# Kernel optimization log

Hardware: AMD Instinct MI355X
Metric: run time of the kernel (lower is better)

Reference implementation:

```python
import jax, jax.numpy as jnp
import numpy as np

LN_EPS = 1e-5
N_HEADS = 8

def _layernorm(x, g, b):
    mu = jnp.mean(x, axis=-1, keepdims=True)
    var = jnp.var(x, axis=-1, keepdims=True)
    return (x - mu) * jax.lax.rsqrt(var + LN_EPS) * g + b

def _posenc(seqlen, d_model, dtype):
    den = jnp.exp(-jnp.arange(0, d_model, 2, dtype=dtype) * (np.log(10000.0) / d_model))
    pos = jnp.arange(seqlen, dtype=dtype)[:, None]  # [S,1]
    pe = jnp.zeros((seqlen, d_model), dtype=dtype)
    pe = pe.at[:, 0::2].set(jnp.sin(pos * den))
    pe = pe.at[:, 1::2].set(jnp.cos(pos * den)[:, : d_model // 2])
    return pe  # [S,d]

def setup_inputs() -> dict:
    key = jax.random.key(0)
    ks = jax.random.split(key, 12)
    B, S, V, D, F, L, DL = 64, 256, 16, 512, 2048, 6, 256
    s = 0.05
    return {
        "src_pad": jax.random.normal(ks[0], (B, S, V), jnp.float32),
        "emb_w": jax.random.normal(ks[1], (D, V), jnp.float32) * s,
        "emb_b": jnp.zeros((D,), jnp.float32),
        "qkv_w": jax.random.normal(ks[2], (L, 3 * D, D), jnp.float32) * s,
        "qkv_b": jnp.zeros((L, 3 * D), jnp.float32),
        "out_w": jax.random.normal(ks[3], (L, D, D), jnp.float32) * s,
        "out_b": jnp.zeros((L, D), jnp.float32),
        "ff1_w": jax.random.normal(ks[4], (L, F, D), jnp.float32) * s,
        "ff1_b": jnp.zeros((L, F), jnp.float32),
        "ff2_w": jax.random.normal(ks[5], (L, D, F), jnp.float32) * s,
        "ff2_b": jnp.zeros((L, D), jnp.float32),
        "ln1_g": jnp.ones((L, D), jnp.float32),
        "ln1_b": jnp.zeros((L, D), jnp.float32),
        "ln2_g": jnp.ones((L, D), jnp.float32),
        "ln2_b": jnp.zeros((L, D), jnp.float32),
        "lat_w": jax.random.normal(ks[6], (DL, S * D), jnp.float32) * 0.005,
        "lat_b": jnp.zeros((DL,), jnp.float32),
        "head_w": jax.random.normal(ks[7], (1, DL), jnp.float32) * s,
        "head_b": jnp.zeros((1,), jnp.float32),
    }

def reference(src_pad, emb_w, emb_b, qkv_w, qkv_b, out_w, out_b,
              ff1_w, ff1_b, ff2_w, ff2_b, ln1_g, ln1_b, ln2_g, ln2_b,
              lat_w, lat_b, head_w, head_b):
    B, S, V = src_pad.shape
    D = emb_w.shape[0]
    L = qkv_w.shape[0]
    H = N_HEADS
    dh = D // H
    # batched replacement of the per-token Python-loop embedding
    x = jnp.einsum('bsv,dv->bsd', src_pad, emb_w) + emb_b
    x = x + _posenc(S, D, x.dtype)  # dropout is identity at eval
    scale = 1.0 / np.sqrt(dh)
    for l in range(L):  # post-norm PyTorch TransformerEncoderLayer, relu FFN
        qkv = jnp.einsum('bsd,ed->bse', x, qkv_w[l]) + qkv_b[l]  # [B,S,3D]
        q, k, v = jnp.split(qkv, 3, axis=-1)
        q = q.reshape(B, S, H, dh).transpose(0, 2, 1, 3)
        k = k.reshape(B, S, H, dh).transpose(0, 2, 1, 3)
        v = v.reshape(B, S, H, dh).transpose(0, 2, 1, 3)
        attn = jax.nn.softmax(jnp.einsum('bhqd,bhkd->bhqk', q, k) * scale, axis=-1)
        o = jnp.einsum('bhqk,bhkd->bhqd', attn, v).transpose(0, 2, 1, 3).reshape(B, S, D)
        o = jnp.einsum('bsd,ed->bse', o, out_w[l]) + out_b[l]
        x = _layernorm(x + o, ln1_g[l], ln1_b[l])
        h = jax.nn.relu(jnp.einsum('bsd,fd->bsf', x, ff1_w[l]) + ff1_b[l])
        h = jnp.einsum('bsf,df->bsd', h, ff2_w[l]) + ff2_b[l]
        x = _layernorm(x + h, ln2_g[l], ln2_b[l])
    mem = x.reshape(B, S * D) @ lat_w.T + lat_b  # [B, d_latent]
    pred = jax.nn.sigmoid(mem @ head_w.T + head_b)  # [B,1]
    return pred
```

## Files before the change

kernel.cpp:

```cpp
#include <hip/hip_runtime.h>
#include <hip/hip_bf16.h>
#include <cstdint>

#define DEV static __device__ __forceinline__

typedef __attribute__((ext_vector_type(8))) short bf16x8;
typedef __attribute__((ext_vector_type(4))) float f32x4;

DEV unsigned short f2bf(float f) {
  union { float f; unsigned u; } c; c.f = f;
  unsigned u = c.u;
  return (unsigned short)((u + 0x7fffu + ((u >> 16) & 1u)) >> 16);
}
DEV float bf2f(unsigned short h) {
  union { unsigned u; float f; } c; c.u = ((unsigned)h) << 16; return c.f;
}
DEV float bflo(unsigned u) { union { unsigned u; float f; } c; c.u = u << 16; return c.f; }
DEV float bfhi(unsigned u) { union { unsigned u; float f; } c; c.u = u & 0xffff0000u; return c.f; }
DEV unsigned pack_bf16(float a, float b) {
  union { float f; unsigned u; } ca, cb; ca.f = a; cb.f = b;
  return __builtin_amdgcn_perm(cb.u + 0x8000u, ca.u + 0x8000u, 0x07060302u);
}

#define ASYNC_COPY16(gsrc, ldst)                                                      \
  __builtin_amdgcn_global_load_lds(                                                   \
      (const __attribute__((address_space(1))) void*)(unsigned long long)(gsrc),      \
      (__attribute__((address_space(3))) void*)(unsigned int)(unsigned long long)(ldst), \
      16, 0, 0)

__global__ void cvt_all_kernel(const float* __restrict__ s0, unsigned short* __restrict__ d0,
                               const float* __restrict__ s1, unsigned short* __restrict__ d1,
                               const float* __restrict__ s2, unsigned short* __restrict__ d2,
                               const float* __restrict__ s3, unsigned short* __restrict__ d3) {
  const int blk = blockIdx.x;
  const float* s; unsigned short* d; int base;
  if (blk < 4608)       { s = s0; d = d0; base = blk; }
  else if (blk < 6144)  { s = s1; d = d1; base = blk - 4608; }
  else if (blk < 12288) { s = s2; d = d2; base = blk - 6144; }
  else                  { s = s3; d = d3; base = blk - 12288; }
  size_t i = ((size_t)base * 256 + threadIdx.x) * 4;
  float4 v = *(const float4*)(s + i);
  d[i + 0] = f2bf(v.x);
  d[i + 1] = f2bf(v.y);
  d[i + 2] = f2bf(v.z);
  d[i + 3] = f2bf(v.w);
}

__global__ void embed_kernel(const float* __restrict__ src,
                             const float* __restrict__ emb_w,
                             const float* __restrict__ emb_b,
                             unsigned short* __restrict__ xb) {
  const int bs = blockIdx.x;
  const int d = threadIdx.x;
  const int s = bs & 255;
  __shared__ float sv[16];
  if (d < 16) sv[d] = src[(size_t)bs * 16 + d];
  __syncthreads();
  const float* wr = emb_w + (size_t)d * 16;
  float acc = emb_b[d];
#pragma unroll
  for (int v = 0; v < 16; v++) acc += sv[v] * wr[v];
  const float den = __expf(-(float)(d & ~1) * (9.2103403719761836f / 512.f));
  const float arg = (float)s * den;
  acc += (d & 1) ? __cosf(arg) : __sinf(arg);
  xb[(size_t)bs * 512 + d] = f2bf(acc);
}

template <int BM, int RELU>
__global__ __launch_bounds__(512, 2) void gemm_pipe(
    const unsigned short* __restrict__ A,
    const unsigned short* __restrict__ B,
    const float* __restrict__ bias,
    unsigned short* __restrict__ Cb,
    int M, int N, int K) {
  constexpr int BN = 256;
  constexpr int MT = BM / 32;
  constexpr int NT = 4;
  constexpr int NLA = BM / 64;
  constexpr int NL = NLA + BN / 64;
  constexpr int BUFE = (BM + BN) * 64;
  __shared__ unsigned short lds[3 * BUFE];

  const int tid = threadIdx.x;
  const int lane = tid & 63;
  const int w = tid >> 6;
  const int wmi = w >> 2;
  const int wni = w & 3;
  const int r16 = lane & 15;
  const int quad = lane >> 4;
  const int rsw = r16 & 7;
  const int m0 = blockIdx.x * BM;
  const int n0 = blockIdx.y * BN;

  const int srow = tid >> 3;
  const int scol = ((tid & 7) ^ (srow & 7)) * 8;
  const unsigned short* gA = A + (size_t)(m0 + srow) * K + scol;
  const unsigned short* gB = B + (size_t)(n0 + srow) * K + scol;

#define STG(i, bufi, kc)                                                        \
  do {                                                                          \
    if ((i) < NLA)                                                              \
      ASYNC_COPY16(gA + (size_t)((i) * 64) * K + (kc),                          \
                   lds + (bufi) * BUFE + ((i) * 64 + w * 8) * 64);              \
    else                                                                        \
      ASYNC_COPY16(gB + (size_t)(((i) - NLA) * 64) * K + (kc),                  \
                   lds + (bufi) * BUFE + (BM + ((i) - NLA) * 64 + w * 8) * 64); \
  } while (0)

  f32x4 acc[MT][NT] = {};

  const int NK = K >> 6;
#pragma unroll
  for (int i = 0; i < NL; ++i) STG(i, 0, 0);
#pragma unroll
  for (int i = 0; i < NL; ++i) STG(i, 1, 64);

  for (int kt = 0; kt < NK; ++kt) {
    const int buf = kt % 3;
    if (kt + 1 < NK)
      asm volatile("s_waitcnt vmcnt(%0)" ::"i"(NL) : "memory");
    else
      asm volatile("s_waitcnt vmcnt(0)" ::: "memory");
    __builtin_amdgcn_s_barrier();
    if (kt + 2 < NK) {
      const int sb = (kt + 2) % 3;
      const int kc = (kt + 2) << 6;
#pragma unroll
      for (int i = 0; i < NL; ++i) STG(i, sb, kc);
    }
    const unsigned short* As = lds + buf * BUFE;
    const unsigned short* Bs = As + BM * 64;
#pragma unroll
    for (int kh = 0; kh < 2; ++kh) {
      const int ko = ((kh * 4 + quad) ^ rsw) * 8;
      bf16x8 aR[MT], bR[NT];
#pragma unroll
      for (int m = 0; m < MT; ++m)
        aR[m] = *(const bf16x8*)(As + (wmi * 64 + m * 16 + r16) * 64 + ko);
#pragma unroll
      for (int j = 0; j < NT; ++j)
        bR[j] = *(const bf16x8*)(Bs + (wni * 64 + j * 16 + r16) * 64 + ko);
      __builtin_amdgcn_s_setprio(1);
#pragma unroll
      for (int m = 0; m < MT; ++m)
#pragma unroll
        for (int j = 0; j < NT; ++j)
          acc[m][j] = __builtin_amdgcn_mfma_f32_16x16x32_bf16(
              bR[j], aR[m], acc[m][j], 0, 0, 0);
      __builtin_amdgcn_s_setprio(0);
    }
    asm volatile("s_waitcnt lgkmcnt(0)" ::: "memory");
  }
#undef STG

  const int mb = m0 + wmi * 64 + r16;
  const int nb = n0 + wni * 64 + quad * 4;
#pragma unroll
  for (int j = 0; j < NT; ++j) {
    const int n = nb + j * 16;
    const float4 bv = *(const float4*)(bias + n);
#pragma unroll
    for (int i = 0; i < MT; ++i) {
      const size_t off = (size_t)(mb + i * 16) * N + n;
      float4 v;
      v.x = acc[i][j][0] + bv.x;
      v.y = acc[i][j][1] + bv.y;
      v.z = acc[i][j][2] + bv.z;
      v.w = acc[i][j][3] + bv.w;
      if (RELU) {
        v.x = fmaxf(v.x, 0.f); v.y = fmaxf(v.y, 0.f);
        v.z = fmaxf(v.z, 0.f); v.w = fmaxf(v.w, 0.f);
      }
      uint2 u;
      u.x = pack_bf16(v.x, v.y);
      u.y = pack_bf16(v.z, v.w);
      *(uint2*)(Cb + off) = u;
    }
  }
}

__global__ __launch_bounds__(512, 2) void gemm_ln(
    const unsigned short* __restrict__ A,
    const unsigned short* __restrict__ B,
    const float* __restrict__ bias,
    const float* __restrict__ g,
    const float* __restrict__ beta,
    unsigned short* __restrict__ xb,
    int K) {
  constexpr int BM = 64;
  constexpr int MT = 4;
  constexpr int NT = 4;
  constexpr int NL = 1 + 8;
  constexpr int BUFE = (BM + 512) * 64;
  __shared__ unsigned short lds[2 * BUFE];

  const int tid = threadIdx.x;
  const int lane = tid & 63;
  const int w = tid >> 6;
  const int r16 = lane & 15;
  const int quad = lane >> 4;
  const int rsw = r16 & 7;
  const int m0 = blockIdx.x * BM;

  const int srow = tid >> 3;
  const int scol = ((tid & 7) ^ (srow & 7)) * 8;
  const unsigned short* gA = A + (size_t)(m0 + srow) * K + scol;
  const unsigned short* gB = B + (size_t)srow * K + scol;

#define STG2(i, bufi, kc)                                                       \
  do {                                                                          \
    if ((i) == 0)                                                               \
      ASYNC_COPY16(gA + (size_t)(kc), lds + (bufi) * BUFE + (w * 8) * 64);      \
    else                                                                        \
      ASYNC_COPY16(gB + (size_t)(((i) - 1) * 64) * K + (kc),                    \
                   lds + (bufi) * BUFE + (BM + ((i) - 1) * 64 + w * 8) * 64);   \
  } while (0)

  f32x4 acc[MT][NT] = {};

  const int NK = K >> 6;
#pragma unroll
  for (int i = 0; i < NL; ++i) STG2(i, 0, 0);

  for (int kt = 0; kt < NK; ++kt) {
    const int buf = kt & 1;
    if (kt + 1 < NK) {
      const int kc = (kt + 1) << 6;
#pragma unroll
      for (int i = 0; i < NL; ++i) STG2(i, buf ^ 1, kc);
      asm volatile("s_waitcnt vmcnt(%0)" ::"i"(NL) : "memory");
    } else {
      asm volatile("s_waitcnt vmcnt(0)" ::: "memory");
    }
    __builtin_amdgcn_s_barrier();
    const unsigned short* As = lds + buf * BUFE;
    const unsigned short* Bs = As + BM * 64;
#pragma unroll
    for (int kh = 0; kh < 2; ++kh) {
      const int ko = ((kh * 4 + quad) ^ rsw) * 8;
      bf16x8 aR[MT], bR[NT];
#pragma unroll
      for (int m = 0; m < MT; ++m)
        aR[m] = *(const bf16x8*)(As + (m * 16 + r16) * 64 + ko);
#pragma unroll
      for (int j = 0; j < NT; ++j)
        bR[j] = *(const bf16x8*)(Bs + (w * 64 + j * 16 + r16) * 64 + ko);
      __builtin_amdgcn_s_setprio(1);
#pragma unroll
      for (int m = 0; m < MT; ++m)
#pragma unroll
        for (int j = 0; j < NT; ++j)
          acc[m][j] = __builtin_amdgcn_mfma_f32_16x16x32_bf16(
              bR[j], aR[m], acc[m][j], 0, 0, 0);
      __builtin_amdgcn_s_setprio(0);
    }
    asm volatile("s_waitcnt lgkmcnt(0)" ::: "memory");
    __builtin_amdgcn_s_barrier();
  }
#undef STG2

  const int nb = w * 64 + quad * 4;
  float psum[MT] = {}, psq[MT] = {};
#pragma unroll
  for (int j = 0; j < NT; ++j) {
    const int n = nb + j * 16;
    const float4 bv = *(const float4*)(bias + n);
#pragma unroll
    for (int i = 0; i < MT; ++i) {
      const size_t off = (size_t)(m0 + i * 16 + r16) * 512 + n;
      const uint2 ru = *(const uint2*)(xb + off);
      f32x4 v;
      v[0] = acc[i][j][0] + bv.x + bflo(ru.x);
      v[1] = acc[i][j][1] + bv.y + bfhi(ru.x);
      v[2] = acc[i][j][2] + bv.z + bflo(ru.y);
      v[3] = acc[i][j][3] + bv.w + bfhi(ru.y);
      acc[i][j] = v;
#pragma unroll
      for (int r = 0; r < 4; ++r) {
        psum[i] += v[r];
        psq[i] += v[r] * v[r];
      }
    }
  }
#pragma unroll
  for (int i = 0; i < MT; ++i) {
    psum[i] += __shfl_xor(psum[i], 16);
    psum[i] += __shfl_xor(psum[i], 32);
    psq[i] += __shfl_xor(psq[i], 16);
    psq[i] += __shfl_xor(psq[i], 32);
  }
  float* redS = (float*)lds;
  float* redQ = redS + 512;
  if (quad == 0) {
#pragma unroll
    for (int i = 0; i < MT; ++i) {
      redS[w * 64 + i * 16 + r16] = psum[i];
      redQ[w * 64 + i * 16 + r16] = psq[i];
    }
  }
  __syncthreads();
  float mu[MT], rs[MT];
#pragma unroll
  for (int i = 0; i < MT; ++i) {
    const int row = i * 16 + r16;
    float s = 0.f, q = 0.f;
#pragma unroll
    for (int ww = 0; ww < 8; ++ww) {
      s += redS[ww * 64 + row];
      q += redQ[ww * 64 + row];
    }
    mu[i] = s * (1.f / 512.f);
    rs[i] = rsqrtf(q * (1.f / 512.f) - mu[i] * mu[i] + 1e-5f);
  }
#pragma unroll
  for (int j = 0; j < NT; ++j) {
    const int n = nb + j * 16;
    const float4 gv = *(const float4*)(g + n);
    const float4 be = *(const float4*)(beta + n);
#pragma unroll
    for (int i = 0; i < MT; ++i) {
      const size_t off = (size_t)(m0 + i * 16 + r16) * 512 + n;
      const f32x4 v = acc[i][j];
      float o0 = (v[0] - mu[i]) * rs[i] * gv.x + be.x;
      float o1 = (v[1] - mu[i]) * rs[i] * gv.y + be.y;
      float o2 = (v[2] - mu[i]) * rs[i] * gv.z + be.z;
      float o3 = (v[3] - mu[i]) * rs[i] * gv.w + be.w;
      uint2 u;
      u.x = pack_bf16(o0, o1);
      u.y = pack_bf16(o2, o3);
      *(uint2*)(xb + off) = u;
    }
  }
}

__global__ __launch_bounds__(256, 2) void attn_fused(
    const unsigned short* __restrict__ qkv,
    unsigned short* __restrict__ O) {
  __shared__ unsigned short Vt[64 * 264];
  __shared__ unsigned short Pl[32 * 264];
  __shared__ float redM[4][32];
  __shared__ float redS[4][32];
  const int tid = threadIdx.x;
  const int lane = tid & 63;
  const int w = tid >> 6;
  const int r16 = lane & 15;
  const int quad = lane >> 4;
  const int h = blockIdx.x & 7;
  const int b = blockIdx.x >> 3;

  {
    const int kp = w * 32 + (lane & 31);
    const int dhalf = lane >> 5;
    const unsigned short* vbase =
        qkv + (size_t)(b * 256 + 2 * kp) * 1536 + 1024 + h * 64;
    unsigned* dst = (unsigned*)Vt;
#pragma unroll
    for (int t = 0; t < 4; t++) {
      const int dc = dhalf + 2 * t;
      const uint4 a = *(const uint4*)(vbase + dc * 8);
      const uint4 bb = *(const uint4*)(vbase + 1536 + dc * 8);
      const unsigned* ap = (const unsigned*)&a;
      const unsigned* bp = (const unsigned*)&bb;
#pragma unroll
      for (int i = 0; i < 4; i++) {
        const unsigned lo = ap[i], hi = bp[i];
        dst[(dc * 8 + 2 * i) * 132 + kp] = (lo & 0xffffu) | (hi << 16);
        dst[(dc * 8 + 2 * i + 1) * 132 + kp] = (lo >> 16) | (hi & 0xffff0000u);
      }
    }
  }
  __syncthreads();

  const unsigned short* krow =
      qkv + (size_t)(b * 256 + r16) * 1536 + 512 + h * 64 + quad * 8;
  const unsigned short* qrow =
      qkv + (size_t)(b * 256 + r16) * 1536 + h * 64 + quad * 8;

  for (int qt = 0; qt < 8; qt++) {
    const int q0 = qt * 32;
    f32x4 acc[4][2] = {};
    bf16x8 bQ0[2], bQ1[2];
#pragma unroll
    for (int nt = 0; nt < 2; nt++) {
      const unsigned short* qp = qrow + (size_t)(q0 + nt * 16) * 1536;
      bQ0[nt] = *(const bf16x8*)(qp);
      bQ1[nt] = *(const bf16x8*)(qp + 32);
    }
#pragma unroll
    for (int mt = 0; mt < 4; mt++) {
      const unsigned short* kp = krow + (size_t)(w * 64 + mt * 16) * 1536;
      const bf16x8 aK0 = *(const bf16x8*)(kp);
      const bf16x8 aK1 = *(const bf16x8*)(kp + 32);
#pragma unroll
      for (int nt = 0; nt < 2; nt++) {
        acc[mt][nt] = __builtin_amdgcn_mfma_f32_16x16x32_bf16(aK0, bQ0[nt], acc[mt][nt], 0, 0, 0);
        acc[mt][nt] = __builtin_amdgcn_mfma_f32_16x16x32_bf16(aK1, bQ1[nt], acc[mt][nt], 0, 0, 0);
      }
    }
    float ml[2];
#pragma unroll
    for (int nt = 0; nt < 2; nt++) {
      float m = acc[0][nt][0];
#pragma unroll
      for (int mt = 0; mt < 4; mt++)
#pragma unroll
        for (int r = 0; r < 4; r++) m = fmaxf(m, acc[mt][nt][r]);
      m = fmaxf(m, __shfl_xor(m, 16));
      m = fmaxf(m, __shfl_xor(m, 32));
      ml[nt] = m;
      float s = 0.f;
#pragma unroll
      for (int mt = 0; mt < 4; mt++)
#pragma unroll
        for (int r = 0; r < 4; r++) {
          acc[mt][nt][r] = __expf((acc[mt][nt][r] - m) * 0.125f);
          s += acc[mt][nt][r];
        }
      s += __shfl_xor(s, 16);
      s += __shfl_xor(s, 32);
      if (quad == 0) {
        redM[w][nt * 16 + r16] = m;
        redS[w][nt * 16 + r16] = s;
      }
    }
    __syncthreads();
    float scale[2];
#pragma unroll
    for (int nt = 0; nt < 2; nt++) {
      const int q = nt * 16 + r16;
      const float m0_ = redM[0][q], m1_ = redM[1][q];
      const float m2_ = redM[2][q], m3_ = redM[3][q];
      const float mg = fmaxf(fmaxf(m0_, m1_), fmaxf(m2_, m3_));
      const float sg = redS[0][q] * __expf((m0_ - mg) * 0.125f) +
                       redS[1][q] * __expf((m1_ - mg) * 0.125f) +
                       redS[2][q] * __expf((m2_ - mg) * 0.125f) +
                       redS[3][q] * __expf((m3_ - mg) * 0.125f);
      scale[nt] = __expf((ml[nt] - mg) * 0.125f) / sg;
    }
#pragma unroll
    for (int nt = 0; nt < 2; nt++) {
      unsigned short* prow = Pl + (nt * 16 + r16) * 264 + w * 64 + quad * 4;
#pragma unroll
      for (int mt = 0; mt < 4; mt++) {
        uint2 u;
        u.x = pack_bf16(acc[mt][nt][0] * scale[nt], acc[mt][nt][1] * scale[nt]);
        u.y = pack_bf16(acc[mt][nt][2] * scale[nt], acc[mt][nt][3] * scale[nt]);
        *(uint2*)(prow + mt * 16) = u;
      }
    }
    __syncthreads();
    f32x4 o[2] = {};
#pragma unroll
    for (int s = 0; s < 8; s++) {
      const bf16x8 aV = *(const bf16x8*)(Vt + (w * 16 + r16) * 264 + s * 32 + quad * 8);
#pragma unroll
      for (int nt = 0; nt < 2; nt++) {
        const bf16x8 bP = *(const bf16x8*)(Pl + (nt * 16 + r16) * 264 + s * 32 + quad * 8);
        o[nt] = __builtin_amdgcn_mfma_f32_16x16x32_bf16(aV, bP, o[nt], 0, 0, 0);
      }
    }
#pragma unroll
    for (int nt = 0; nt < 2; nt++) {
      uint2 u;
      u.x = pack_bf16(o[nt][0], o[nt][1]);
      u.y = pack_bf16(o[nt][2], o[nt][3]);
      *(uint2*)(O + (size_t)(b * 256 + q0 + nt * 16 + r16) * 512 + h * 64 +
                w * 16 + quad * 4) = u;
    }
  }
}

__global__ void zero_kernel(float* __restrict__ p) {
  p[blockIdx.x * 256 + threadIdx.x] = 0.f;
}

__global__ __launch_bounds__(256) void latent_gemm(
    const unsigned short* __restrict__ xb, const float* __restrict__ W,
    float* __restrict__ mem) {
  const int tid = threadIdx.x;
  const int lane = tid & 63;
  const int w = tid >> 6;
  const int r16 = lane & 15;
  const int quad = lane >> 4;
  const int n0 = blockIdx.x * 64 + w * 16;
  const int kc0 = blockIdx.y * 1024;

  const float* wrow = W + (size_t)(n0 + r16) * 131072 + kc0 + quad * 8;
  const unsigned short* xrow = xb + (size_t)r16 * 131072 + kc0 + quad * 8;

  f32x4 c[4] = {};
  for (int k = 0; k < 1024; k += 32) {
    const float4 wa = *(const float4*)(wrow + k);
    const float4 wb = *(const float4*)(wrow + k + 4);
    union { unsigned u[4]; bf16x8 v; } cw;
    cw.u[0] = pack_bf16(wa.x, wa.y);
    cw.u[1] = pack_bf16(wa.z, wa.w);
    cw.u[2] = pack_bf16(wb.x, wb.y);
    cw.u[3] = pack_bf16(wb.z, wb.w);
#pragma unroll
    for (int i = 0; i < 4; i++) {
      const bf16x8 aX = *(const bf16x8*)(xrow + (size_t)i * 2097152 + k);
      c[i] = __builtin_amdgcn_mfma_f32_16x16x32_bf16(aX, cw.v, c[i], 0, 0, 0);
    }
  }
#pragma unroll
  for (int i = 0; i < 4; i++)
#pragma unroll
    for (int r = 0; r < 4; r++)
      atomicAdd(&mem[(size_t)(i * 16 + quad * 4 + r) * 256 + n0 + r16], c[i][r]);
}

__global__ __launch_bounds__(256) void head_kernel(
    const float* __restrict__ mem, const float* __restrict__ lat_b,
    const float* __restrict__ head_w, const float* __restrict__ head_b,
    float* __restrict__ out) {
  const int b = blockIdx.x;
  const int tid = threadIdx.x;
  float v = (mem[(size_t)b * 256 + tid] + lat_b[tid]) * head_w[tid];
#pragma unroll
  for (int off = 32; off > 0; off >>= 1) v += __shfl_xor(v, off);
  __shared__ float red[4];
  const int w = tid >> 6, lane = tid & 63;
  if (lane == 0) red[w] = v;
  __syncthreads();
  if (tid == 0) {
    const float z = red[0] + red[1] + red[2] + red[3] + head_b[0];
    out[b] = 1.f / (1.f + __expf(-z));
  }
}

extern "C" void kernel_launch(void* const* d_in, const int* in_sizes, int n_in,
                              void* d_out, int out_size, void* d_ws, size_t ws_size,
                              hipStream_t stream) {
  (void)in_sizes; (void)n_in; (void)out_size; (void)ws_size;
  const float* src_pad = (const float*)d_in[0];
  const float* emb_w = (const float*)d_in[1];
  const float* emb_b = (const float*)d_in[2];
  const float* qkv_w = (const float*)d_in[3];
  const float* qkv_b = (const float*)d_in[4];
  const float* out_w = (const float*)d_in[5];
  const float* out_b = (const float*)d_in[6];
  const float* ff1_w = (const float*)d_in[7];
  const float* ff1_b = (const float*)d_in[8];
  const float* ff2_w = (const float*)d_in[9];
  const float* ff2_b = (const float*)d_in[10];
  const float* ln1_g = (const float*)d_in[11];
  const float* ln1_b = (const float*)d_in[12];
  const float* ln2_g = (const float*)d_in[13];
  const float* ln2_b = (const float*)d_in[14];
  const float* lat_w = (const float*)d_in[15];
  const float* lat_b = (const float*)d_in[16];
  const float* head_w = (const float*)d_in[17];
  const float* head_b = (const float*)d_in[18];
  float* out = (float*)d_out;

  char* p = (char*)d_ws;
  unsigned short* xb = (unsigned short*)p; p += (size_t)16384 * 512 * 2;
  unsigned short* qkv = (unsigned short*)p; p += (size_t)16384 * 1536 * 2;
  unsigned short* attno = (unsigned short*)p; p += (size_t)16384 * 512 * 2;
  unsigned short* h = (unsigned short*)p;     p += (size_t)16384 * 2048 * 2;
  unsigned short* wq = (unsigned short*)p;    p += (size_t)4718592 * 2;
  unsigned short* wo = (unsigned short*)p;    p += (size_t)1572864 * 2;
  unsigned short* wf1 = (unsigned short*)p;   p += (size_t)6291456 * 2;
  unsigned short* wf2 = (unsigned short*)p;   p += (size_t)6291456 * 2;
  float* mem = (float*)p;           p += (size_t)16384 * 4;

  cvt_all_kernel<<<18432, 256, 0, stream>>>(qkv_w, wq, out_w, wo, ff1_w, wf1,
                                            ff2_w, wf2);

  embed_kernel<<<16384, 512, 0, stream>>>(src_pad, emb_w, emb_b, xb);

  for (int l = 0; l < 6; l++) {
    gemm_pipe<128, 0><<<dim3(128, 6), 512, 0, stream>>>(
        xb, wq + (size_t)l * 786432, qkv_b + (size_t)l * 1536, qkv,
        16384, 1536, 512);
    attn_fused<<<512, 256, 0, stream>>>(qkv, attno);
    gemm_ln<<<256, 512, 0, stream>>>(
        attno, wo + (size_t)l * 262144, out_b + (size_t)l * 512,
        ln1_g + (size_t)l * 512, ln1_b + (size_t)l * 512, xb, 512);
    gemm_pipe<128, 1><<<dim3(128, 8), 512, 0, stream>>>(
        xb, wf1 + (size_t)l * 1048576, ff1_b + (size_t)l * 2048, h,
        16384, 2048, 512);
    gemm_ln<<<256, 512, 0, stream>>>(
        h, wf2 + (size_t)l * 1048576, ff2_b + (size_t)l * 512,
        ln2_g + (size_t)l * 512, ln2_b + (size_t)l * 512, xb, 2048);
  }

  zero_kernel<<<64, 256, 0, stream>>>(mem);
  latent_gemm<<<dim3(4, 128), 256, 0, stream>>>(xb, lat_w, mem);
  head_kernel<<<64, 256, 0, stream>>>(mem, lat_b, head_w, head_b, out);
}
```

Measured before the change: 1.511 ms.

## Replace triple-buffered 128x256 GEMM with simple single-buffered 128x128 GEMM

Replaces the pipelined GEMM with a simpler kernel for the QKV and FF1 projections. The old kernel used three LDS stages and async prefetch two tiles ahead over a 128x256 tile with 512 threads. The new kernel uses a 128x128 tile, 256 threads and a single LDS buffer that is loaded, waited on and synchronised every k-step. The intent is higher occupancy and more blocks, at the cost of losing the overlap of global loads with MFMA work and getting less reuse of A per block.

Result: faster. 1.477 ms (-2.3%).

```diff
diff --git a/kernel.cpp b/kernel.cpp
--- a/kernel.cpp
+++ b/kernel.cpp
@@ -66,101 +66,74 @@
   xb[(size_t)bs * 512 + d] = f2bf(acc);
 }
 
-template <int BM, int RELU>
-__global__ __launch_bounds__(512, 2) void gemm_pipe(
+template <int RELU>
+__global__ __launch_bounds__(256, 3) void gemm_nt(
     const unsigned short* __restrict__ A,
     const unsigned short* __restrict__ B,
     const float* __restrict__ bias,
     unsigned short* __restrict__ Cb,
     int M, int N, int K) {
-  constexpr int BN = 256;
-  constexpr int MT = BM / 32;
+  constexpr int MT = 4;
   constexpr int NT = 4;
-  constexpr int NLA = BM / 64;
-  constexpr int NL = NLA + BN / 64;
-  constexpr int BUFE = (BM + BN) * 64;
-  __shared__ unsigned short lds[3 * BUFE];
-
+  __shared__ unsigned short As[128 * 64];
+  __shared__ unsigned short Bs[128 * 64];
   const int tid = threadIdx.x;
   const int lane = tid & 63;
   const int w = tid >> 6;
-  const int wmi = w >> 2;
-  const int wni = w & 3;
+  const int m0 = blockIdx.x * 128;
+  const int n0 = blockIdx.y * 128;
+
+  const int srow = lane >> 3;
+  const int scol = (((lane & 7) ^ srow)) * 8;
+  const unsigned short* gA0 = A + (size_t)(m0 + w * 32 + srow) * K + scol;
+  unsigned short* lA0 = As + (w * 32) * 64;
+  const unsigned short* gB0 = B + (size_t)(n0 + w * 32 + srow) * K + scol;
+  unsigned short* lB0 = Bs + (w * 32) * 64;
+
+  const int wm = (w >> 1) * 64;
+  const int wn = (w & 1) * 64;
   const int r16 = lane & 15;
   const int quad = lane >> 4;
   const int rsw = r16 & 7;
-  const int m0 = blockIdx.x * BM;
-  const int n0 = blockIdx.y * BN;
-
-  const int srow = tid >> 3;
-  const int scol = ((tid & 7) ^ (srow & 7)) * 8;
-  const unsigned short* gA = A + (size_t)(m0 + srow) * K + scol;
-  const unsigned short* gB = B + (size_t)(n0 + srow) * K + scol;
-
-#define STG(i, bufi, kc)                                                        \
-  do {                                                                          \
-    if ((i) < NLA)                                                              \
-      ASYNC_COPY16(gA + (size_t)((i) * 64) * K + (kc),                          \
-                   lds + (bufi) * BUFE + ((i) * 64 + w * 8) * 64);              \
-    else                                                                        \
-      ASYNC_COPY16(gB + (size_t)(((i) - NLA) * 64) * K + (kc),                  \
-                   lds + (bufi) * BUFE + (BM + ((i) - NLA) * 64 + w * 8) * 64); \
-  } while (0)
 
   f32x4 acc[MT][NT] = {};
 
-  const int NK = K >> 6;
-#pragma unroll
-  for (int i = 0; i < NL; ++i) STG(i, 0, 0);
-#pragma unroll
-  for (int i = 0; i < NL; ++i) STG(i, 1, 64);
-
-  for (int kt = 0; kt < NK; ++kt) {
-    const int buf = kt % 3;
-    if (kt + 1 < NK)
-      asm volatile("s_waitcnt vmcnt(%0)" ::"i"(NL) : "memory");
-    else
-      asm volatile("s_waitcnt vmcnt(0)" ::: "memory");
-    __builtin_amdgcn_s_barrier();
-    if (kt + 2 < NK) {
-      const int sb = (kt + 2) % 3;
-      const int kc = (kt + 2) << 6;
-#pragma unroll
-      for (int i = 0; i < NL; ++i) STG(i, sb, kc);
-    }
-    const unsigned short* As = lds + buf * BUFE;
-    const unsigned short* Bs = As + BM * 64;
-#pragma unroll
-    for (int kh = 0; kh < 2; ++kh) {
+  for (int k0 = 0; k0 < K; k0 += 64) {
+#pragma unroll
+    for (int i = 0; i < 4; i++)
+      ASYNC_COPY16(gA0 + (size_t)(i * 8) * K + k0, lA0 + i * 512);
+#pragma unroll
+    for (int i = 0; i < 4; i++)
+      ASYNC_COPY16(gB0 + (size_t)(i * 8) * K + k0, lB0 + i * 512);
+    asm volatile("s_waitcnt vmcnt(0)" ::: "memory");
+    __syncthreads();
+#pragma unroll
+    for (int kh = 0; kh < 2; kh++) {
       const int ko = ((kh * 4 + quad) ^ rsw) * 8;
-      bf16x8 aR[MT], bR[NT];
-#pragma unroll
-      for (int m = 0; m < MT; ++m)
-        aR[m] = *(const bf16x8*)(As + (wmi * 64 + m * 16 + r16) * 64 + ko);
-#pragma unroll
-      for (int j = 0; j < NT; ++j)
-        bR[j] = *(const bf16x8*)(Bs + (wni * 64 + j * 16 + r16) * 64 + ko);
-      __builtin_amdgcn_s_setprio(1);
-#pragma unroll
-      for (int m = 0; m < MT; ++m)
-#pragma unroll
-        for (int j = 0; j < NT; ++j)
-          acc[m][j] = __builtin_amdgcn_mfma_f32_16x16x32_bf16(
-              bR[j], aR[m], acc[m][j], 0, 0, 0);
-      __builtin_amdgcn_s_setprio(0);
-    }
-    asm volatile("s_waitcnt lgkmcnt(0)" ::: "memory");
-  }
-#undef STG
-
-  const int mb = m0 + wmi * 64 + r16;
-  const int nb = n0 + wni * 64 + quad * 4;
-#pragma unroll
-  for (int j = 0; j < NT; ++j) {
+      bf16x8 xa[MT], wb[NT];
+#pragma unroll
+      for (int i = 0; i < MT; i++)
+        xa[i] = *(const bf16x8*)(As + (wm + i * 16 + r16) * 64 + ko);
+#pragma unroll
+      for (int j = 0; j < NT; j++)
+        wb[j] = *(const bf16x8*)(Bs + (wn + j * 16 + r16) * 64 + ko);
+#pragma unroll
+      for (int i = 0; i < MT; i++)
+#pragma unroll
+        for (int j = 0; j < NT; j++)
+          acc[i][j] = __builtin_amdgcn_mfma_f32_16x16x32_bf16(wb[j], xa[i], acc[i][j], 0, 0, 0);
+    }
+    __syncthreads();
+  }
+
+  const int mb = m0 + wm + r16;
+  const int nb = n0 + wn + quad * 4;
+#pragma unroll
+  for (int j = 0; j < NT; j++) {
     const int n = nb + j * 16;
     const float4 bv = *(const float4*)(bias + n);
 #pragma unroll
-    for (int i = 0; i < MT; ++i) {
+    for (int i = 0; i < MT; i++) {
       const size_t off = (size_t)(mb + i * 16) * N + n;
       float4 v;
       v.x = acc[i][j][0] + bv.x;
@@ -571,14 +544,14 @@
   embed_kernel<<<16384, 512, 0, stream>>>(src_pad, emb_w, emb_b, xb);
 
   for (int l = 0; l < 6; l++) {
-    gemm_pipe<128, 0><<<dim3(128, 6), 512, 0, stream>>>(
+    gemm_nt<0><<<dim3(128, 12), 256, 0, stream>>>(
         xb, wq + (size_t)l * 786432, qkv_b + (size_t)l * 1536, qkv,
         16384, 1536, 512);
     attn_fused<<<512, 256, 0, stream>>>(qkv, attno);
     gemm_ln<<<256, 512, 0, stream>>>(
         attno, wo + (size_t)l * 262144, out_b + (size_t)l * 512,
         ln1_g + (size_t)l * 512, ln1_b + (size_t)l * 512, xb, 512);
-    gemm_pipe<128, 1><<<dim3(128, 8), 512, 0, stream>>>(
+    gemm_nt<1><<<dim3(128, 16), 256, 0, stream>>>(
         xb, wf1 + (size_t)l * 1048576, ff1_b + (size_t)l * 2048, h,
         16384, 2048, 512);
     gemm_ln<<<256, 512, 0, stream>>>(
```
